# Kernel tuning notes

Measured on AMD Instinct MI355X. Metric: run time of the kernel, lower is better.

The kernel has to match this reference:

```python
import jax, jax.numpy as jnp
import numpy as np

S, M, B, D, H, DH = 1024, 1024, 4, 1024, 16, 64
T = S + M


def _rel_shift(x):
    # x: [i, j, b, n] -> Transformer-XL relative shift
    i, j = x.shape[0], x.shape[1]
    zero_pad = jnp.zeros((i, 1) + x.shape[2:], x.dtype)
    x_padded = jnp.concatenate([zero_pad, x], axis=1)
    x_padded = x_padded.reshape((j + 1, i) + x.shape[2:])
    return x_padded[1:].reshape(x.shape)


def setup_inputs() -> dict:
    key = jax.random.key(0)
    ks = jax.random.split(key, 8)
    sc = 0.02
    x = jax.random.normal(ks[0], (S, B, D), jnp.float32)
    memory = jax.random.normal(ks[1], (M, B, D), jnp.float32)
    pos_emb = jax.random.normal(ks[2], (T, D), jnp.float32)
    pos_bias_u = jax.random.normal(ks[3], (H, DH), jnp.float32) * sc
    pos_bias_v = jax.random.normal(ks[4], (H, DH), jnp.float32) * sc
    W_qkv = jax.random.normal(ks[5], (D, 3 * H * DH), jnp.float32) * sc
    W_rel = jax.random.normal(ks[6], (D, H * DH), jnp.float32) * sc
    W_o = jax.random.normal(ks[7], (H * DH, D), jnp.float32) * sc
    gamma = jnp.ones((D,), jnp.float32)
    beta = jnp.zeros((D,), jnp.float32)
    # causal mask accounting for memory: query i attends keys j <= i + M
    causal = jnp.arange(T)[None, :] > (jnp.arange(S)[:, None] + M)
    mask = jnp.broadcast_to(causal[:, :, None], (S, T, B))
    return {"x": x, "pos_emb": pos_emb, "pos_bias_u": pos_bias_u,
            "pos_bias_v": pos_bias_v, "memory": memory,
            "W_qkv": W_qkv, "W_rel": W_rel, "W_o": W_o,
            "gamma": gamma, "beta": beta, "mask": mask}


def reference(x, pos_emb, pos_bias_u, pos_bias_v, memory, W_qkv, W_rel, W_o, gamma, beta, mask):
    seq_len, batch, d_model = x.shape
    num_head, d_head = pos_bias_u.shape
    scale = 1.0 / d_head ** 0.5

    c = jnp.concatenate([memory, x], axis=0)          # [T, B, D]
    total_len = c.shape[0]

    qkv = c @ W_qkv                                   # [T, B, 3*H*DH]
    q, k, v = jnp.split(qkv, 3, axis=-1)
    q = q.reshape(total_len, batch, num_head, d_head)[-seq_len:]  # [S,B,H,DH]
    k = k.reshape(total_len, batch, num_head, d_head)             # [T,B,H,DH]
    v = v.reshape(total_len, batch, num_head, d_head)             # [T,B,H,DH]
    r = (pos_emb @ W_rel).reshape(total_len, num_head, d_head)    # [T,H,DH]

    AC = jnp.einsum('ibnd,jbnd->ijbn', q + pos_bias_u, k)  # content-content
    BD = jnp.einsum('ibnd,jnd->ijbn', q + pos_bias_v, r)   # content-position
    BD = _rel_shift(BD)

    attn_score = (AC + BD) * scale                    # [S,T,B,H]
    attn_score = jnp.where(mask[:, :, :, None], -jnp.inf, attn_score)
    attn_prob = jax.nn.softmax(attn_score, axis=1)

    attn_vec = jnp.einsum('ijbn,jbnd->ibnd', attn_prob, v)
    attn_vec = attn_vec.reshape(seq_len, batch, num_head * d_head)
    attn_out = attn_vec @ W_o                         # [S,B,D]

    y = x + attn_out
    mu = jnp.mean(y, axis=-1, keepdims=True)
    var = jnp.var(y, axis=-1, keepdims=True)
    return (y - mu) / jnp.sqrt(var + 1e-5) * gamma + beta
```

## Files before the change

kernel.cpp:

```cpp
#include <hip/hip_runtime.h>
#include <math.h>
#include <cstdint>
#include <cstddef>


typedef _Float16 half_t;
typedef _Float16 half8 __attribute__((ext_vector_type(8)));
typedef _Float16 half4v __attribute__((ext_vector_type(4)));
typedef float f32x4 __attribute__((ext_vector_type(4)));

#define S_LEN 1024
#define M_LEN 1024
#define T_LEN 2048
#define BATCH 4
#define NHEAD 16

__device__ inline void async_copy16(const half_t* g, half_t* l) {
  __builtin_amdgcn_global_load_lds(
      (const __attribute__((address_space(1))) void*)g,
      (__attribute__((address_space(3))) void*)l, 16, 0, 0);
}

__global__ __launch_bounds__(256) void k_pre(const float* __restrict__ mem,
                                             const float* __restrict__ x,
                                             const float* __restrict__ pos,
                                             const float* __restrict__ Wqkv,
                                             const float* __restrict__ Wrel,
                                             const float* __restrict__ Wo,
                                             half_t* __restrict__ cbf,
                                             half_t* __restrict__ posb,
                                             half_t* __restrict__ wqkvT,
                                             half_t* __restrict__ wrelT,
                                             half_t* __restrict__ woT) {
  __shared__ float tile[64][65];
  const int bid = blockIdx.x;
  const int t = threadIdx.x;
  if (bid < 10240) {
    const int i = bid * 256 + t;
    if (i < 2097152) {
      const int off = i & 1048575;
      const int sel = i >> 20;
      const float4 v = ((const float4*)(sel ? x : mem))[off];
      const int row = off >> 8, d4 = off & 255;
      const int drow = (row & 3) * 2048 + sel * 1024 + (row >> 2);
      half4v h;
      h[0] = (half_t)v.x; h[1] = (half_t)v.y; h[2] = (half_t)v.z; h[3] = (half_t)v.w;
      ((half4v*)cbf)[(drow << 8) + d4] = h;
    } else {
      const int off = i - 2097152;
      const float4 v = ((const float4*)pos)[off];
      half4v h;
      h[0] = (half_t)v.x; h[1] = (half_t)v.y; h[2] = (half_t)v.z; h[3] = (half_t)v.w;
      ((half4v*)posb)[off] = h;
    }
    return;
  }
  const int tb = bid - 10240;
  const int bx = tb & 15, y = tb >> 4;
  const float* src; half_t* dst; int C, c0;
  if (y < 48)      { src = Wqkv; dst = wqkvT; C = 3072; c0 = y * 64; }
  else if (y < 64) { src = Wrel; dst = wrelT; C = 1024; c0 = (y - 48) * 64; }
  else             { src = Wo;   dst = woT;   C = 1024; c0 = (y - 64) * 64; }
  const int r0 = bx * 64;
  const int tx = t & 63, ty4 = t >> 6;
#pragma unroll
  for (int k = 0; k < 16; ++k) {
    int row = k * 4 + ty4;
    tile[row][tx] = src[(size_t)(r0 + row) * C + c0 + tx];
  }
  __syncthreads();
#pragma unroll
  for (int k = 0; k < 16; ++k) {
    int orow = k * 4 + ty4;
    dst[(size_t)(c0 + orow) * 1024 + r0 + tx] = (half_t)tile[tx][orow];
  }
}

#define QP_STAGE(buf_, k0_)                                                    \
  do {                                                                         \
    _Pragma("unroll") for (int i_ = 0; i_ < 4; ++i_) {                         \
      const int r0_ = wave * 32 + i_ * 8;                                      \
      async_copy16(&A[(size_t)(m0 + r0_ + srw) * 1024 + (k0_) + scl],          \
                   &ldsA[buf_][r0_][0]);                                       \
      async_copy16(&B[(size_t)(n0 + r0_ + srw) * 1024 + (k0_) + scl],          \
                   &ldsB[buf_][r0_][0]);                                       \
    }                                                                          \
  } while (0)

#define QP_COMPUTE(d_)                                                         \
  do {                                                                         \
    _Pragma("unroll") for (int ks_ = 0; ks_ < 2; ++ks_) {                      \
      half8 bf_[4];                                                            \
      _Pragma("unroll") for (int nt_ = 0; nt_ < 4; ++nt_) {                    \
        const int rw_ = wn + nt_ * 16 + l15;                                   \
        bf_[nt_] =                                                             \
            *(const half8*)&ldsB[d_][rw_][((ks_ * 4 + quad) ^ (rw_ & 7)) * 8]; \
      }                                                                        \
      half8 af_[8];                                                            \
      _Pragma("unroll") for (int mt_ = 0; mt_ < 8; ++mt_) {                    \
        const int rw_ = wm + mt_ * 16 + l15;                                   \
        af_[mt_] =                                                             \
            *(const half8*)&ldsA[d_][rw_][((ks_ * 4 + quad) ^ (rw_ & 7)) * 8]; \
      }                                                                        \
      __builtin_amdgcn_s_setprio(1);                                           \
      _Pragma("unroll") for (int mt_ = 0; mt_ < 8; ++mt_)                      \
        _Pragma("unroll") for (int nt_ = 0; nt_ < 4; ++nt_)                    \
          acc[mt_][nt_] = __builtin_amdgcn_mfma_f32_16x16x32_f16(              \
              af_[mt_], bf_[nt_], acc[mt_][nt_], 0, 0, 0);                     \
      __builtin_amdgcn_s_setprio(0);                                           \
    }                                                                          \
  } while (0)

__global__ __launch_bounds__(512, 2) void k_gemm_qkv_pos(const half_t* __restrict__ cbf,
                                                         const half_t* __restrict__ wqkvT,
                                                         half_t* __restrict__ qkv,
                                                         const half_t* __restrict__ posb,
                                                         const half_t* __restrict__ wrelT,
                                                         half_t* __restrict__ rb,
                                                         half_t* __restrict__ vT) {
  __shared__ half_t ldsA[2][256][64];
  __shared__ half_t ldsB[2][256][64];
  const int t = threadIdx.x;
  const int wave = t >> 6, lane = t & 63, quad = lane >> 4, l15 = lane & 15;
  const int bid0 = blockIdx.x;
  const int bid = (bid0 & 7) * 52 + (bid0 >> 3);
  const half_t* A; const half_t* B; half_t* C; int m0, n0, N;
  if (bid < 256) {
    A = cbf;  B = wqkvT; C = qkv; N = 2048;
    m0 = (bid & 31) * 256; n0 = (bid >> 5) * 256;
  } else if (bid < 384) {
    const int b2 = bid - 256;
    A = wqkvT + 2048 * 1024; B = cbf; C = vT; N = 8192;
    m0 = (b2 & 3) * 256; n0 = (b2 >> 2) * 256;
  } else {
    const int b2 = bid - 384;
    A = posb; B = wrelT; C = rb; N = 1024;
    m0 = (b2 & 7) * 256; n0 = (b2 >> 3) * 256;
  }
  const int srw = lane >> 3;
  const int scl = ((lane & 7) ^ srw) * 8;
  const int wm = (wave >> 2) * 128, wn = (wave & 3) * 64;

  f32x4 acc[8][4] = {};

  QP_STAGE(0, 0);
  __syncthreads();
  int d = 0;
  for (int kt = 0; kt < 15; ++kt) {
    QP_STAGE(d ^ 1, (kt + 1) * 64);
    QP_COMPUTE(d);
    __syncthreads();
    d ^= 1;
  }
  QP_COMPUTE(d);

#pragma unroll
  for (int mt = 0; mt < 8; ++mt)
#pragma unroll
    for (int nt = 0; nt < 4; ++nt)
#pragma unroll
      for (int r = 0; r < 4; ++r)
        C[(size_t)(m0 + wm + mt * 16 + quad * 4 + r) * N + n0 + wn + nt * 16 + l15] =
            (half_t)acc[mt][nt][r];
}

#define PJ_STAGE(buf_, k0_)                                                    \
  do {                                                                         \
    _Pragma("unroll") for (int i_ = 0; i_ < 2; ++i_) {                         \
      const int r0_ = wave * 16 + i_ * 8;                                      \
      async_copy16(&A[(size_t)(m0 + r0_ + srw) * 1024 + (k0_) + scl],          \
                   &pA[buf_][r0_][0]);                                         \
    }                                                                          \
    _Pragma("unroll") for (int i_ = 0; i_ < 4; ++i_) {                         \
      const int r0_ = wave * 32 + i_ * 8;                                      \
      async_copy16(&B[(size_t)(n0 + r0_ + srw) * 1024 + (k0_) + scl],          \
                   &pB[buf_][r0_][0]);                                         \
    }                                                                          \
  } while (0)

#define PJ_COMPUTE(d_)                                                         \
  do {                                                                         \
    _Pragma("unroll") for (int ks_ = 0; ks_ < 2; ++ks_) {                      \
      half8 bf_[4];                                                            \
      _Pragma("unroll") for (int nt_ = 0; nt_ < 4; ++nt_) {                    \
        const int rw_ = wn + nt_ * 16 + l15;                                   \
        bf_[nt_] =                                                             \
            *(const half8*)&pB[d_][rw_][((ks_ * 4 + quad) ^ (rw_ & 7)) * 8];   \
      }                                                                        \
      half8 af_[4];                                                            \
      _Pragma("unroll") for (int mt_ = 0; mt_ < 4; ++mt_) {                    \
        const int rw_ = wm + mt_ * 16 + l15;                                   \
        af_[mt_] =                                                             \
            *(const half8*)&pA[d_][rw_][((ks_ * 4 + quad) ^ (rw_ & 7)) * 8];   \
      }                                                                        \
      __builtin_amdgcn_s_setprio(1);                                           \
      _Pragma("unroll") for (int mt_ = 0; mt_ < 4; ++mt_)                      \
        _Pragma("unroll") for (int nt_ = 0; nt_ < 4; ++nt_)                    \
          acc[mt_][nt_] = __builtin_amdgcn_mfma_f32_16x16x32_f16(              \
              af_[mt_], bf_[nt_], acc[mt_][nt_], 0, 0, 0);                     \
      __builtin_amdgcn_s_setprio(0);                                           \
    }                                                                          \
  } while (0)

__global__ __launch_bounds__(512, 2) void k_gemm_proj(const half_t* __restrict__ av,
                                                      const half_t* __restrict__ woT,
                                                      half_t* __restrict__ out0,
                                                      half_t* __restrict__ out1) {
  __shared__ half_t pA[2][128][64];
  __shared__ half_t pB[2][256][64];
  const int t = threadIdx.x;
  const int wave = t >> 6, lane = t & 63, quad = lane >> 4, l15 = lane & 15;
  const int bid0 = blockIdx.x;
  const int bs = (bid0 & 7) * 32 + (bid0 >> 3);
  const int h = bs >> 7, b2 = bs & 127;
  const int m0 = (b2 & 31) * 128, n0 = (b2 >> 5) * 256;
  const half_t* A = av + h * 512;
  const half_t* B = woT + h * 512;
  half_t* C = h ? out1 : out0;
  const int srw = lane >> 3;
  const int scl = ((lane & 7) ^ srw) * 8;
  const int wm = (wave >> 2) * 64, wn = (wave & 3) * 64;

  f32x4 acc[4][4] = {};

  PJ_STAGE(0, 0);
  __syncthreads();
  int d = 0;
  for (int kt = 0; kt < 7; ++kt) {
    PJ_STAGE(d ^ 1, (kt + 1) * 64);
    PJ_COMPUTE(d);
    __syncthreads();
    d ^= 1;
  }
  PJ_COMPUTE(d);

#pragma unroll
  for (int mt = 0; mt < 4; ++mt)
#pragma unroll
    for (int nt = 0; nt < 4; ++nt)
#pragma unroll
      for (int r = 0; r < 4; ++r)
        C[(size_t)(m0 + wm + mt * 16 + quad * 4 + r) * 1024 + n0 + wn + nt * 16 + l15] =
            (half_t)acc[mt][nt][r];
}

__global__ __launch_bounds__(512, 4) void k_attn(const half_t* __restrict__ qkv,
                                                 const half_t* __restrict__ rbuf,
                                                 const half_t* __restrict__ vT,
                                                 const float* __restrict__ pbu,
                                                 const float* __restrict__ pbv,
                                                 half_t* __restrict__ av) {
  __shared__ __align__(16) half_t ldsK[64][64];
  __shared__ __align__(16) half_t ldsV[64][64];
  __shared__ __align__(16) half_t ldsR[256][64];
  __shared__ __align__(16) half_t ldsP[8][16][72];
  const int t = threadIdx.x;
  const int wave = t >> 6, lane = t & 63, quad = lane >> 4, l15 = lane & 15;

  const int li = blockIdx.x + 8 * blockIdx.y;
  const int c = li & 255, kr = li >> 8;
  const int xe = kr == 0 ? (c & 7) : 7 - (c & 7);
  const int bn = (c >> 3) + (kr << 5);
  const int i0 = xe * 128;
  const int b = bn >> 4, n = bn & 15;
  const int i_base = i0 + wave * 16;
  const int p0 = 896 - i0;

  half8 qu[2], qv[2];
#pragma unroll
  for (int ks = 0; ks < 2; ++ks) {
    const int dh0 = ks * 32 + quad * 8;
    const half8 qf = *(const half8*)&qkv[((size_t)(b * 2048 + M_LEN + i_base + l15)) * 2048 + n * 64 + dh0];
#pragma unroll
    for (int j = 0; j < 8; ++j) {
      const float qj = (float)qf[j];
      qu[ks][j] = (half_t)(qj + pbu[n * 64 + dh0 + j]);
      qv[ks][j] = (half_t)(qj + pbv[n * 64 + dh0 + j]);
    }
  }

  int bperm_idx[4];
  bool lo_sel[4];
#pragma unroll
  for (int r = 0; r < 4; ++r) {
    const int irow = quad * 4 + r;
    bperm_idx[r] = ((lane & 48) | ((l15 + 15 - irow) & 15)) << 2;
    lo_sel[r] = (l15 <= irow);
  }

  f32x4 oacc[4] = {};
  float lpart[4] = {0.f, 0.f, 0.f, 0.f};
  const float k1 = 0.125f * 1.44269504088896f;
  const float kC = -4.0f * 1.44269504088896f;

  const int srow = t >> 3, sc3 = t & 7;
  const int sxk = (sc3 ^ (srow & 7)) * 8;

  const int ntile = xe * 2 + 18;

  half8 kreg = *(const half8*)&qkv[((size_t)(b * 2048 + srow)) * 2048 + 1024 + n * 64 + sc3 * 8];
  half8 vreg = *(const half8*)&vT[((size_t)(n * 64 + srow)) * 8192 + b * 2048 + sc3 * 8];
  half8 rreg4[4];
  int rr4[4], rc4[4];
#pragma unroll
  for (int i = 0; i < 4; ++i) {
    const int ci = t + 512 * i;
    rr4[i] = ci >> 3; rc4[i] = ci & 7;
    const int ps = p0 + rr4[i] > 2047 ? 2047 : p0 + rr4[i];
    rreg4[i] = *(const half8*)&rbuf[(size_t)ps * 1024 + n * 64 + rc4[i] * 8];
  }
  half8 rpre;

  for (int kt = 0; kt < ntile; ++kt) {
    const int j0 = kt * 64;

    __syncthreads();
    *(half8*)&ldsK[srow][sxk] = kreg;
    *(half8*)&ldsV[srow][sxk] = vreg;
    if (kt == 0) {
#pragma unroll
      for (int i = 0; i < 4; ++i) {
        const int pg = p0 + rr4[i];
        *(half8*)&ldsR[pg & 255][(rc4[i] ^ (pg & 7)) * 8] = rreg4[i];
      }
    } else {
      const int pw = j0 + p0 + 192 + srow;
      *(half8*)&ldsR[pw & 255][(sc3 ^ (pw & 7)) * 8] = rpre;
    }
    __syncthreads();

    if (kt + 1 < ntile) {
      const int j0n = j0 + 64;
      kreg = *(const half8*)&qkv[((size_t)(b * 2048 + j0n + srow)) * 2048 + 1024 + n * 64 + sc3 * 8];
      vreg = *(const half8*)&vT[((size_t)(n * 64 + srow)) * 8192 + b * 2048 + j0n + sc3 * 8];
      const int pn = j0 + p0 + 256 + srow;
      const int pc = pn > 2047 ? 2047 : pn;
      rpre = *(const half8*)&rbuf[(size_t)pc * 1024 + n * 64 + sc3 * 8];
    }

    f32x4 ac[4] = {};
#pragma unroll
    for (int ks = 0; ks < 2; ++ks)
#pragma unroll
      for (int nt = 0; nt < 4; ++nt) {
        const int row = nt * 16 + l15;
        const half8 kf = *(const half8*)&ldsK[row][((ks * 4 + quad) ^ (row & 7)) * 8];
        ac[nt] = __builtin_amdgcn_mfma_f32_16x16x32_f16(qu[ks], kf, ac[nt], 0, 0, 0);
      }

    const int rbg = j0 + p0 + 112 - wave * 16;
    f32x4 ea[5] = {};
#pragma unroll
    for (int ks = 0; ks < 2; ++ks)
#pragma unroll
      for (int et = 0; et < 5; ++et) {
        const int pr = rbg + et * 16 + l15;
        const half8 rf = *(const half8*)&ldsR[pr & 255][((ks * 4 + quad) ^ (pr & 7)) * 8];
        ea[et] = __builtin_amdgcn_mfma_f32_16x16x32_f16(qv[ks], rf, ea[et], 0, 0, 0);
      }

    const bool maskt = j0 > i_base + 960;
#pragma unroll
    for (int r = 0; r < 4; ++r) {
      const int irow = quad * 4 + r;
      const int ig = i_base + irow;
      float rot[5];
#pragma unroll
      for (int et = 0; et < 5; ++et)
        rot[et] = __int_as_float(
            __builtin_amdgcn_ds_bpermute(bperm_idx[r], __float_as_int(ea[et][r])));
      float psum = 0.f;
#pragma unroll
      for (int nt = 0; nt < 4; ++nt) {
        const float ev = lo_sel[r] ? rot[nt] : rot[nt + 1];
        const int cj = nt * 16 + l15;
        float p = __builtin_amdgcn_exp2f(fmaf(ac[nt][r] + ev, k1, kC));
        if (maskt && (j0 + cj > ig + M_LEN)) p = 0.f;
        psum += p;
        ldsP[wave][irow][cj] = (half_t)p;
      }
      lpart[r] += psum;
    }
    __builtin_amdgcn_wave_barrier();

    half8 pa[2];
#pragma unroll
    for (int ks = 0; ks < 2; ++ks)
      pa[ks] = *(const half8*)&ldsP[wave][l15][ks * 32 + quad * 8];
#pragma unroll
    for (int ks = 0; ks < 2; ++ks)
#pragma unroll
      for (int dnt = 0; dnt < 4; ++dnt) {
        const int row = dnt * 16 + l15;
        const half8 vf = *(const half8*)&ldsV[row][((ks * 4 + quad) ^ (row & 7)) * 8];
        oacc[dnt] = __builtin_amdgcn_mfma_f32_16x16x32_f16(pa[ks], vf, oacc[dnt], 0, 0, 0);
      }
  }

#pragma unroll
  for (int r = 0; r < 4; ++r) {
    float l = lpart[r];
#pragma unroll
    for (int off = 1; off < 16; off <<= 1) l += __shfl_xor(l, off);
    const float inv = 1.0f / l;
    const int ig = i_base + quad * 4 + r;
#pragma unroll
    for (int dnt = 0; dnt < 4; ++dnt)
      av[((size_t)ig * BATCH + b) * 1024 + n * 64 + dnt * 16 + l15] = (half_t)(oacc[dnt][r] * inv);
  }
}

__global__ __launch_bounds__(256) void k_ln(const float* __restrict__ x,
                                            const half_t* __restrict__ ao0,
                                            const half_t* __restrict__ ao1,
                                            const float* __restrict__ gamma,
                                            const float* __restrict__ beta,
                                            float* __restrict__ out) {
  const int row = blockIdx.x;
  const int t = threadIdx.x;
  const float4 xv = ((const float4*)(x + (size_t)row * 1024))[t];
  const half4v a4 = ((const half4v*)(ao0 + (size_t)row * 1024))[t];
  const half4v b4 = ((const half4v*)(ao1 + (size_t)row * 1024))[t];
  const float y0 = xv.x + (float)a4[0] + (float)b4[0];
  const float y1 = xv.y + (float)a4[1] + (float)b4[1];
  const float y2 = xv.z + (float)a4[2] + (float)b4[2];
  const float y3 = xv.w + (float)a4[3] + (float)b4[3];
  float s = y0 + y1 + y2 + y3;
  float ss = y0 * y0 + y1 * y1 + y2 * y2 + y3 * y3;
#pragma unroll
  for (int off = 1; off < 64; off <<= 1) {
    s += __shfl_xor(s, off);
    ss += __shfl_xor(ss, off);
  }
  __shared__ float sb[4], ssb[4];
  if ((t & 63) == 0) { sb[t >> 6] = s; ssb[t >> 6] = ss; }
  __syncthreads();
  s = sb[0] + sb[1] + sb[2] + sb[3];
  ss = ssb[0] + ssb[1] + ssb[2] + ssb[3];
  const float mean = s * (1.f / 1024.f);
  const float var = ss * (1.f / 1024.f) - mean * mean;
  const float rstd = rsqrtf(var + 1e-5f);
  const float4 g = ((const float4*)gamma)[t];
  const float4 be = ((const float4*)beta)[t];
  float4 o;
  o.x = (y0 - mean) * rstd * g.x + be.x;
  o.y = (y1 - mean) * rstd * g.y + be.y;
  o.z = (y2 - mean) * rstd * g.z + be.z;
  o.w = (y3 - mean) * rstd * g.w + be.w;
  ((float4*)(out + (size_t)row * 1024))[t] = o;
}

extern "C" void kernel_launch(void* const* d_in, const int* in_sizes, int n_in,
                              void* d_out, int out_size, void* d_ws, size_t ws_size,
                              hipStream_t stream) {
  const float* x     = (const float*)d_in[0];
  const float* pos   = (const float*)d_in[1];
  const float* pbu   = (const float*)d_in[2];
  const float* pbv   = (const float*)d_in[3];
  const float* mem   = (const float*)d_in[4];
  const float* Wqkv  = (const float*)d_in[5];
  const float* Wrel  = (const float*)d_in[6];
  const float* Wo    = (const float*)d_in[7];
  const float* gamma = (const float*)d_in[8];
  const float* beta  = (const float*)d_in[9];
  float* out = (float*)d_out;

  half_t* ws    = (half_t*)d_ws;
  half_t* cbf   = ws;
  half_t* posb  = cbf + 8388608;
  half_t* wqkvT = posb + 2097152;
  half_t* wrelT = wqkvT + 3145728;
  half_t* woT   = wrelT + 1048576;
  half_t* qkv   = woT + 1048576;
  half_t* rb    = qkv + 16777216;
  half_t* vT    = rb + 2097152;
  half_t* av    = vT + 8388608;
  half_t* aout0 = qkv;
  half_t* aout1 = qkv + 4194304;

  k_pre<<<11520, 256, 0, stream>>>(mem, x, pos, Wqkv, Wrel, Wo, cbf, posb, wqkvT, wrelT, woT);
  k_gemm_qkv_pos<<<416, 512, 0, stream>>>(cbf, wqkvT, qkv, posb, wrelT, rb, vT);
  k_attn<<<dim3(8, 64), 512, 0, stream>>>(qkv, rb, vT, pbu, pbv, av);
  k_gemm_proj<<<256, 512, 0, stream>>>(av, woT, aout0, aout1);
  k_ln<<<4096, 256, 0, stream>>>(x, aout0, aout1, gamma, beta, out);
}
```

Baseline: 310.7 us.

## Give each attention wave two query row tiles with 256-thread blocks

The attention kernel now runs 4 waves per block instead of 8, and each wave handles two 16-row query tiles. The K, V and R fragments read from LDS are shared across both tiles, and the R fragments of adjacent tiles overlap, so one set of six R loads feeds both. This cuts LDS reads per MFMA and the number of waves taking part in block barriers. s_setprio is added around the MFMA sections. The cost is higher register pressure from doubled accumulators and fewer waves available to hide latency.

```diff
diff --git a/kernel.cpp b/kernel.cpp
--- a/kernel.cpp
+++ b/kernel.cpp
@@ -244,7 +244,7 @@
             (half_t)acc[mt][nt][r];
 }
 
-__global__ __launch_bounds__(512, 4) void k_attn(const half_t* __restrict__ qkv,
+__global__ __launch_bounds__(256, 2) void k_attn(const half_t* __restrict__ qkv,
                                                  const half_t* __restrict__ rbuf,
                                                  const half_t* __restrict__ vT,
                                                  const float* __restrict__ pbu,
@@ -253,7 +253,7 @@
   __shared__ __align__(16) half_t ldsK[64][64];
   __shared__ __align__(16) half_t ldsV[64][64];
   __shared__ __align__(16) half_t ldsR[256][64];
-  __shared__ __align__(16) half_t ldsP[8][16][72];
+  __shared__ __align__(16) half_t ldsP[4][2][16][72];
   const int t = threadIdx.x;
   const int wave = t >> 6, lane = t & 63, quad = lane >> 4, l15 = lane & 15;
 
@@ -263,21 +263,23 @@
   const int bn = (c >> 3) + (kr << 5);
   const int i0 = xe * 128;
   const int b = bn >> 4, n = bn & 15;
-  const int i_base = i0 + wave * 16;
   const int p0 = 896 - i0;
 
-  half8 qu[2], qv[2];
-#pragma unroll
-  for (int ks = 0; ks < 2; ++ks) {
-    const int dh0 = ks * 32 + quad * 8;
-    const half8 qf = *(const half8*)&qkv[((size_t)(b * 2048 + M_LEN + i_base + l15)) * 2048 + n * 64 + dh0];
-#pragma unroll
-    for (int j = 0; j < 8; ++j) {
-      const float qj = (float)qf[j];
-      qu[ks][j] = (half_t)(qj + pbu[n * 64 + dh0 + j]);
-      qv[ks][j] = (half_t)(qj + pbv[n * 64 + dh0 + j]);
-    }
-  }
+  half8 qu[2][2], qv[2][2];
+#pragma unroll
+  for (int hi = 0; hi < 2; ++hi)
+#pragma unroll
+    for (int ks = 0; ks < 2; ++ks) {
+      const int dh0 = ks * 32 + quad * 8;
+      const int ig = i0 + (wave * 2 + hi) * 16 + l15;
+      const half8 qf = *(const half8*)&qkv[((size_t)(b * 2048 + M_LEN + ig)) * 2048 + n * 64 + dh0];
+#pragma unroll
+      for (int j = 0; j < 8; ++j) {
+        const float qj = (float)qf[j];
+        qu[hi][ks][j] = (half_t)(qj + pbu[n * 64 + dh0 + j]);
+        qv[hi][ks][j] = (half_t)(qj + pbv[n * 64 + dh0 + j]);
+      }
+    }
 
   int bperm_idx[4];
   bool lo_sel[4];
@@ -288,126 +290,150 @@
     lo_sel[r] = (l15 <= irow);
   }
 
-  f32x4 oacc[4] = {};
-  float lpart[4] = {0.f, 0.f, 0.f, 0.f};
+  f32x4 oacc[2][4] = {};
+  float lpart[2][4] = {};
   const float k1 = 0.125f * 1.44269504088896f;
   const float kC = -4.0f * 1.44269504088896f;
 
-  const int srow = t >> 3, sc3 = t & 7;
-  const int sxk = (sc3 ^ (srow & 7)) * 8;
+  const int sr = t >> 3, sc3 = t & 7;
+  const int sxk = (sc3 ^ (sr & 7)) * 8;
 
   const int ntile = xe * 2 + 18;
 
-  half8 kreg = *(const half8*)&qkv[((size_t)(b * 2048 + srow)) * 2048 + 1024 + n * 64 + sc3 * 8];
-  half8 vreg = *(const half8*)&vT[((size_t)(n * 64 + srow)) * 8192 + b * 2048 + sc3 * 8];
-  half8 rreg4[4];
-  int rr4[4], rc4[4];
-#pragma unroll
-  for (int i = 0; i < 4; ++i) {
-    const int ci = t + 512 * i;
-    rr4[i] = ci >> 3; rc4[i] = ci & 7;
-    const int ps = p0 + rr4[i] > 2047 ? 2047 : p0 + rr4[i];
-    rreg4[i] = *(const half8*)&rbuf[(size_t)ps * 1024 + n * 64 + rc4[i] * 8];
-  }
-  half8 rpre;
+#pragma unroll
+  for (int i = 0; i < 8; ++i) {
+    const int rr = i * 32 + sr;
+    const int pg = p0 + rr;
+    const int ps = pg > 2047 ? 2047 : pg;
+    const half8 rv = *(const half8*)&rbuf[(size_t)ps * 1024 + n * 64 + sc3 * 8];
+    *(half8*)&ldsR[pg & 255][(sc3 ^ (pg & 7)) * 8] = rv;
+  }
+  half8 kreg0 = *(const half8*)&qkv[((size_t)(b * 2048 + sr)) * 2048 + 1024 + n * 64 + sc3 * 8];
+  half8 kreg1 = *(const half8*)&qkv[((size_t)(b * 2048 + sr + 32)) * 2048 + 1024 + n * 64 + sc3 * 8];
+  half8 vreg0 = *(const half8*)&vT[((size_t)(n * 64 + sr)) * 8192 + b * 2048 + sc3 * 8];
+  half8 vreg1 = *(const half8*)&vT[((size_t)(n * 64 + sr + 32)) * 8192 + b * 2048 + sc3 * 8];
+  half8 rpre0, rpre1;
 
   for (int kt = 0; kt < ntile; ++kt) {
     const int j0 = kt * 64;
 
     __syncthreads();
-    *(half8*)&ldsK[srow][sxk] = kreg;
-    *(half8*)&ldsV[srow][sxk] = vreg;
-    if (kt == 0) {
-#pragma unroll
-      for (int i = 0; i < 4; ++i) {
-        const int pg = p0 + rr4[i];
-        *(half8*)&ldsR[pg & 255][(rc4[i] ^ (pg & 7)) * 8] = rreg4[i];
-      }
-    } else {
-      const int pw = j0 + p0 + 192 + srow;
-      *(half8*)&ldsR[pw & 255][(sc3 ^ (pw & 7)) * 8] = rpre;
+    *(half8*)&ldsK[sr][sxk] = kreg0;
+    *(half8*)&ldsK[sr + 32][sxk] = kreg1;
+    *(half8*)&ldsV[sr][sxk] = vreg0;
+    *(half8*)&ldsV[sr + 32][sxk] = vreg1;
+    if (kt > 0) {
+      const int pw0 = j0 + p0 + 192 + sr;
+      *(half8*)&ldsR[pw0 & 255][(sc3 ^ (pw0 & 7)) * 8] = rpre0;
+      const int pw1 = pw0 + 32;
+      *(half8*)&ldsR[pw1 & 255][(sc3 ^ (pw1 & 7)) * 8] = rpre1;
     }
     __syncthreads();
 
     if (kt + 1 < ntile) {
       const int j0n = j0 + 64;
-      kreg = *(const half8*)&qkv[((size_t)(b * 2048 + j0n + srow)) * 2048 + 1024 + n * 64 + sc3 * 8];
-      vreg = *(const half8*)&vT[((size_t)(n * 64 + srow)) * 8192 + b * 2048 + j0n + sc3 * 8];
-      const int pn = j0 + p0 + 256 + srow;
-      const int pc = pn > 2047 ? 2047 : pn;
-      rpre = *(const half8*)&rbuf[(size_t)pc * 1024 + n * 64 + sc3 * 8];
-    }
-
-    f32x4 ac[4] = {};
+      kreg0 = *(const half8*)&qkv[((size_t)(b * 2048 + j0n + sr)) * 2048 + 1024 + n * 64 + sc3 * 8];
+      kreg1 = *(const half8*)&qkv[((size_t)(b * 2048 + j0n + sr + 32)) * 2048 + 1024 + n * 64 + sc3 * 8];
+      vreg0 = *(const half8*)&vT[((size_t)(n * 64 + sr)) * 8192 + b * 2048 + j0n + sc3 * 8];
+      vreg1 = *(const half8*)&vT[((size_t)(n * 64 + sr + 32)) * 8192 + b * 2048 + j0n + sc3 * 8];
+      const int pn0 = j0 + p0 + 256 + sr;
+      const int pc0 = pn0 > 2047 ? 2047 : pn0;
+      rpre0 = *(const half8*)&rbuf[(size_t)pc0 * 1024 + n * 64 + sc3 * 8];
+      const int pn1 = pn0 + 32;
+      const int pc1 = pn1 > 2047 ? 2047 : pn1;
+      rpre1 = *(const half8*)&rbuf[(size_t)pc1 * 1024 + n * 64 + sc3 * 8];
+    }
+
+    f32x4 ac[2][4] = {};
+    f32x4 ea[2][5] = {};
+    __builtin_amdgcn_s_setprio(1);
 #pragma unroll
     for (int ks = 0; ks < 2; ++ks)
 #pragma unroll
       for (int nt = 0; nt < 4; ++nt) {
         const int row = nt * 16 + l15;
         const half8 kf = *(const half8*)&ldsK[row][((ks * 4 + quad) ^ (row & 7)) * 8];
-        ac[nt] = __builtin_amdgcn_mfma_f32_16x16x32_f16(qu[ks], kf, ac[nt], 0, 0, 0);
+        ac[0][nt] = __builtin_amdgcn_mfma_f32_16x16x32_f16(qu[0][ks], kf, ac[0][nt], 0, 0, 0);
+        ac[1][nt] = __builtin_amdgcn_mfma_f32_16x16x32_f16(qu[1][ks], kf, ac[1][nt], 0, 0, 0);
       }
 
-    const int rbg = j0 + p0 + 112 - wave * 16;
-    f32x4 ea[5] = {};
-#pragma unroll
-    for (int ks = 0; ks < 2; ++ks)
+    const int rbgU = j0 + p0 + 112 - (wave * 2 + 1) * 16;
+#pragma unroll
+    for (int ks = 0; ks < 2; ++ks) {
+      half8 rf[6];
+#pragma unroll
+      for (int u = 0; u < 6; ++u) {
+        const int pr = rbgU + u * 16 + l15;
+        rf[u] = *(const half8*)&ldsR[pr & 255][((ks * 4 + quad) ^ (pr & 7)) * 8];
+      }
 #pragma unroll
       for (int et = 0; et < 5; ++et) {
-        const int pr = rbg + et * 16 + l15;
-        const half8 rf = *(const half8*)&ldsR[pr & 255][((ks * 4 + quad) ^ (pr & 7)) * 8];
-        ea[et] = __builtin_amdgcn_mfma_f32_16x16x32_f16(qv[ks], rf, ea[et], 0, 0, 0);
+        ea[0][et] = __builtin_amdgcn_mfma_f32_16x16x32_f16(qv[0][ks], rf[et + 1], ea[0][et], 0, 0, 0);
+        ea[1][et] = __builtin_amdgcn_mfma_f32_16x16x32_f16(qv[1][ks], rf[et], ea[1][et], 0, 0, 0);
       }
-
-    const bool maskt = j0 > i_base + 960;
-#pragma unroll
-    for (int r = 0; r < 4; ++r) {
-      const int irow = quad * 4 + r;
-      const int ig = i_base + irow;
-      float rot[5];
-#pragma unroll
-      for (int et = 0; et < 5; ++et)
-        rot[et] = __int_as_float(
-            __builtin_amdgcn_ds_bpermute(bperm_idx[r], __float_as_int(ea[et][r])));
-      float psum = 0.f;
-#pragma unroll
-      for (int nt = 0; nt < 4; ++nt) {
-        const float ev = lo_sel[r] ? rot[nt] : rot[nt + 1];
-        const int cj = nt * 16 + l15;
-        float p = __builtin_amdgcn_exp2f(fmaf(ac[nt][r] + ev, k1, kC));
-        if (maskt && (j0 + cj > ig + M_LEN)) p = 0.f;
-        psum += p;
-        ldsP[wave][irow][cj] = (half_t)p;
+    }
+    __builtin_amdgcn_s_setprio(0);
+
+#pragma unroll
+    for (int hi = 0; hi < 2; ++hi) {
+      const int ibg = i0 + (wave * 2 + hi) * 16;
+      const bool maskt = j0 > ibg + 960;
+#pragma unroll
+      for (int r = 0; r < 4; ++r) {
+        const int irow = quad * 4 + r;
+        const int ig = ibg + irow;
+        float rot[5];
+#pragma unroll
+        for (int et = 0; et < 5; ++et)
+          rot[et] = __int_as_float(
+              __builtin_amdgcn_ds_bpermute(bperm_idx[r], __float_as_int(ea[hi][et][r])));
+        float psum = 0.f;
+#pragma unroll
+        for (int nt = 0; nt < 4; ++nt) {
+          const float ev = lo_sel[r] ? rot[nt] : rot[nt + 1];
+          const int cj = nt * 16 + l15;
+          float p = __builtin_amdgcn_exp2f(fmaf(ac[hi][nt][r] + ev, k1, kC));
+          if (maskt && (j0 + cj > ig + M_LEN)) p = 0.f;
+          psum += p;
+          ldsP[wave][hi][irow][cj] = (half_t)p;
+        }
+        lpart[hi][r] += psum;
       }
-      lpart[r] += psum;
     }
     __builtin_amdgcn_wave_barrier();
 
-    half8 pa[2];
-#pragma unroll
-    for (int ks = 0; ks < 2; ++ks)
-      pa[ks] = *(const half8*)&ldsP[wave][l15][ks * 32 + quad * 8];
+    half8 pa0[2], pa1[2];
+#pragma unroll
+    for (int ks = 0; ks < 2; ++ks) {
+      pa0[ks] = *(const half8*)&ldsP[wave][0][l15][ks * 32 + quad * 8];
+      pa1[ks] = *(const half8*)&ldsP[wave][1][l15][ks * 32 + quad * 8];
+    }
+    __builtin_amdgcn_s_setprio(1);
 #pragma unroll
     for (int ks = 0; ks < 2; ++ks)
 #pragma unroll
       for (int dnt = 0; dnt < 4; ++dnt) {
         const int row = dnt * 16 + l15;
         const half8 vf = *(const half8*)&ldsV[row][((ks * 4 + quad) ^ (row & 7)) * 8];
-        oacc[dnt] = __builtin_amdgcn_mfma_f32_16x16x32_f16(pa[ks], vf, oacc[dnt], 0, 0, 0);
+        oacc[0][dnt] = __builtin_amdgcn_mfma_f32_16x16x32_f16(pa0[ks], vf, oacc[0][dnt], 0, 0, 0);
+        oacc[1][dnt] = __builtin_amdgcn_mfma_f32_16x16x32_f16(pa1[ks], vf, oacc[1][dnt], 0, 0, 0);
       }
-  }
-
-#pragma unroll
-  for (int r = 0; r < 4; ++r) {
-    float l = lpart[r];
-#pragma unroll
-    for (int off = 1; off < 16; off <<= 1) l += __shfl_xor(l, off);
-    const float inv = 1.0f / l;
-    const int ig = i_base + quad * 4 + r;
-#pragma unroll
-    for (int dnt = 0; dnt < 4; ++dnt)
-      av[((size_t)ig * BATCH + b) * 1024 + n * 64 + dnt * 16 + l15] = (half_t)(oacc[dnt][r] * inv);
-  }
+    __builtin_amdgcn_s_setprio(0);
+  }
+
+#pragma unroll
+  for (int hi = 0; hi < 2; ++hi)
+#pragma unroll
+    for (int r = 0; r < 4; ++r) {
+      float l = lpart[hi][r];
+#pragma unroll
+      for (int off = 1; off < 16; off <<= 1) l += __shfl_xor(l, off);
+      const float inv = 1.0f / l;
+      const int ig = i0 + (wave * 2 + hi) * 16 + quad * 4 + r;
+#pragma unroll
+      for (int dnt = 0; dnt < 4; ++dnt)
+        av[((size_t)ig * BATCH + b) * 1024 + n * 64 + dnt * 16 + l15] = (half_t)(oacc[hi][dnt][r] * inv);
+    }
 }
 
 __global__ __launch_bounds__(256) void k_ln(const float* __restrict__ x,
@@ -480,7 +506,7 @@
 
   k_pre<<<11520, 256, 0, stream>>>(mem, x, pos, Wqkv, Wrel, Wo, cbf, posb, wqkvT, wrelT, woT);
   k_gemm_qkv_pos<<<416, 512, 0, stream>>>(cbf, wqkvT, qkv, posb, wrelT, rb, vT);
-  k_attn<<<dim3(8, 64), 512, 0, stream>>>(qkv, rb, vT, pbu, pbv, av);
+  k_attn<<<dim3(8, 64), 256, 0, stream>>>(qkv, rb, vT, pbu, pbv, av);
   k_gemm_proj<<<256, 512, 0, stream>>>(av, woT, aout0, aout1);
   k_ln<<<4096, 256, 0, stream>>>(x, aout0, aout1, gamma, beta, out);
 }
```

Result: slower. 325.1 us (+4.6%).

## Restructure QKV/pos GEMM main loop into a fine-grained staged load/MFMA pipeline

Applied to the files above, without the earlier changes.

Replaces the simple double-buffered K loop of the fused QKV/position GEMM with a schedule that splits the 256x256 tile into 128-row halves. Fragment loads, async global-to-LDS copies for upcoming tiles, and four quarter MFMA blocks are interleaved and separated by explicit barriers. A manual vmcnt wait replaces the full syncthreads. The aim is to hide global-load latency and LDS reads behind MFMA work. In exchange it adds many barriers per iteration. It also issues prefetches past the last K tile in the final iterations, which read beyond the row's K extent.

```diff
diff --git a/kernel.cpp b/kernel.cpp
--- a/kernel.cpp
+++ b/kernel.cpp
@@ -76,39 +76,57 @@
   }
 }
 
-#define QP_STAGE(buf_, k0_)                                                    \
-  do {                                                                         \
-    _Pragma("unroll") for (int i_ = 0; i_ < 4; ++i_) {                         \
-      const int r0_ = wave * 32 + i_ * 8;                                      \
-      async_copy16(&A[(size_t)(m0 + r0_ + srw) * 1024 + (k0_) + scl],          \
-                   &ldsA[buf_][r0_][0]);                                       \
-      async_copy16(&B[(size_t)(n0 + r0_ + srw) * 1024 + (k0_) + scl],          \
-                   &ldsB[buf_][r0_][0]);                                       \
+#define QK_STA(tile_, h_)                                                      \
+  do {                                                                         \
+    _Pragma("unroll") for (int i_ = 0; i_ < 2; ++i_) {                         \
+      const int r_ = (t >> 3) + i_ * 64;                                       \
+      async_copy16(&A[(size_t)(m0 + (h_) * 128 + r_) * 1024 +                  \
+                      (tile_) * 64 + scl],                                     \
+                   &sA[(tile_) & 1][h_][r_][(t & 7) * 8]);                     \
     }                                                                          \
   } while (0)
 
-#define QP_COMPUTE(d_)                                                         \
-  do {                                                                         \
-    _Pragma("unroll") for (int ks_ = 0; ks_ < 2; ++ks_) {                      \
-      half8 bf_[4];                                                            \
-      _Pragma("unroll") for (int nt_ = 0; nt_ < 4; ++nt_) {                    \
-        const int rw_ = wn + nt_ * 16 + l15;                                   \
-        bf_[nt_] =                                                             \
-            *(const half8*)&ldsB[d_][rw_][((ks_ * 4 + quad) ^ (rw_ & 7)) * 8]; \
+#define QK_STB(tile_, h_)                                                      \
+  do {                                                                         \
+    _Pragma("unroll") for (int i_ = 0; i_ < 2; ++i_) {                         \
+      const int r_ = (t >> 3) + i_ * 64;                                       \
+      async_copy16(&B[(size_t)(n0 + (h_) * 128 + r_) * 1024 +                  \
+                      (tile_) * 64 + scl],                                     \
+                   &sB[(tile_) & 1][h_][r_][(t & 7) * 8]);                     \
+    }                                                                          \
+  } while (0)
+
+#define QK_LDA(d_, mq_)                                                        \
+  do {                                                                         \
+    _Pragma("unroll") for (int mt_ = 0; mt_ < 4; ++mt_)                        \
+      _Pragma("unroll") for (int ks_ = 0; ks_ < 2; ++ks_) {                    \
+        const int lr_ = ((mq_) * 4 + mt_) * 16 + l15;                          \
+        af[mt_][ks_] = *(const half8*)&sA[d_][wha][lr_]                        \
+                           [((ks_ * 4 + quad) ^ (lr_ & 7)) * 8];               \
       }                                                                        \
-      half8 af_[8];                                                            \
-      _Pragma("unroll") for (int mt_ = 0; mt_ < 8; ++mt_) {                    \
-        const int rw_ = wm + mt_ * 16 + l15;                                   \
-        af_[mt_] =                                                             \
-            *(const half8*)&ldsA[d_][rw_][((ks_ * 4 + quad) ^ (rw_ & 7)) * 8]; \
+  } while (0)
+
+#define QK_LDB(d_, nh_)                                                        \
+  do {                                                                         \
+    _Pragma("unroll") for (int ntl_ = 0; ntl_ < 2; ++ntl_)                     \
+      _Pragma("unroll") for (int ks_ = 0; ks_ < 2; ++ks_) {                    \
+        const int lr_ = wnl + ((nh_) * 2 + ntl_) * 16 + l15;                   \
+        bf[nh_][ntl_][ks_] = *(const half8*)&sB[d_][whb][lr_]                  \
+                                 [((ks_ * 4 + quad) ^ (lr_ & 7)) * 8];         \
       }                                                                        \
-      __builtin_amdgcn_s_setprio(1);                                           \
-      _Pragma("unroll") for (int mt_ = 0; mt_ < 8; ++mt_)                      \
-        _Pragma("unroll") for (int nt_ = 0; nt_ < 4; ++nt_)                    \
-          acc[mt_][nt_] = __builtin_amdgcn_mfma_f32_16x16x32_f16(              \
-              af_[mt_], bf_[nt_], acc[mt_][nt_], 0, 0, 0);                     \
-      __builtin_amdgcn_s_setprio(0);                                           \
-    }                                                                          \
+  } while (0)
+
+#define QK_MMA(mq_, nh_)                                                       \
+  do {                                                                         \
+    __builtin_amdgcn_s_setprio(1);                                             \
+    _Pragma("unroll") for (int mt_ = 0; mt_ < 4; ++mt_)                        \
+      _Pragma("unroll") for (int ntl_ = 0; ntl_ < 2; ++ntl_)                   \
+        _Pragma("unroll") for (int ks_ = 0; ks_ < 2; ++ks_)                    \
+          acc[(mq_) * 4 + mt_][(nh_) * 2 + ntl_] =                             \
+              __builtin_amdgcn_mfma_f32_16x16x32_f16(                          \
+                  af[mt_][ks_], bf[nh_][ntl_][ks_],                            \
+                  acc[(mq_) * 4 + mt_][(nh_) * 2 + ntl_], 0, 0, 0);            \
+    __builtin_amdgcn_s_setprio(0);                                             \
   } while (0)
 
 __global__ __launch_bounds__(512, 2) void k_gemm_qkv_pos(const half_t* __restrict__ cbf,
@@ -118,8 +136,8 @@
                                                          const half_t* __restrict__ wrelT,
                                                          half_t* __restrict__ rb,
                                                          half_t* __restrict__ vT) {
-  __shared__ half_t ldsA[2][256][64];
-  __shared__ half_t ldsB[2][256][64];
+  __shared__ half_t sA[2][2][128][64];
+  __shared__ half_t sB[2][2][128][64];
   const int t = threadIdx.x;
   const int wave = t >> 6, lane = t & 63, quad = lane >> 4, l15 = lane & 15;
   const int bid0 = blockIdx.x;
@@ -137,22 +155,37 @@
     A = posb; B = wrelT; C = rb; N = 1024;
     m0 = (b2 & 7) * 256; n0 = (b2 >> 3) * 256;
   }
-  const int srw = lane >> 3;
-  const int scl = ((lane & 7) ^ srw) * 8;
+  const int scl = ((t & 7) ^ ((t >> 3) & 7)) * 8;
   const int wm = (wave >> 2) * 128, wn = (wave & 3) * 64;
+  const int wha = wave >> 2;
+  const int whb = (wave & 3) >> 1;
+  const int wnl = (wave & 1) * 64;
 
   f32x4 acc[8][4] = {};
-
-  QP_STAGE(0, 0);
-  __syncthreads();
-  int d = 0;
-  for (int kt = 0; kt < 15; ++kt) {
-    QP_STAGE(d ^ 1, (kt + 1) * 64);
-    QP_COMPUTE(d);
-    __syncthreads();
-    d ^= 1;
-  }
-  QP_COMPUTE(d);
+  half8 af[4][2], bf[2][2][2];
+
+  QK_STA(0, 0); QK_STA(0, 1); QK_STB(0, 0); QK_STB(0, 1); QK_STA(1, 0);
+
+  for (int kt = 0; kt < 16; ++kt) {
+    const int d = kt & 1;
+    asm volatile("s_waitcnt vmcnt(2)" ::: "memory");
+    __builtin_amdgcn_s_barrier();
+    QK_LDA(d, 0); QK_LDB(d, 0); QK_STA(kt + 1, 1);
+    __builtin_amdgcn_s_barrier();
+    QK_MMA(0, 0);
+    __builtin_amdgcn_s_barrier();
+    QK_LDB(d, 1); QK_STB(kt + 1, 0);
+    __builtin_amdgcn_s_barrier();
+    QK_MMA(0, 1);
+    __builtin_amdgcn_s_barrier();
+    QK_LDA(d, 1); QK_STB(kt + 1, 1);
+    __builtin_amdgcn_s_barrier();
+    QK_MMA(1, 0);
+    __builtin_amdgcn_s_barrier();
+    QK_STA(kt + 2, 0);
+    __builtin_amdgcn_s_barrier();
+    QK_MMA(1, 1);
+  }
 
 #pragma unroll
   for (int mt = 0; mt < 8; ++mt)
```

Result: no change. 309.1 us (-0.5%).
